# Performance work log

Hardware: AMD Instinct MI355X
Metric: run time of the kernel (lower is better)

The kernel has to match this reference:

```python
import jax, jax.numpy as jnp
import numpy as np

IN_CH = 512
MAX_MID = 512


def setup_inputs() -> dict:
    key = jax.random.key(0)
    k0, k1, k2, k3, k4 = jax.random.split(key, 5)
    B, C, H, W = 32, IN_CH, 64, 64
    x = jax.random.normal(k0, (B, C, H, W), dtype=jnp.float32)
    # torch.nn.Linear params: weight [out, in], bias [out]
    s1 = 1.0 / np.sqrt(C)
    w1 = jax.random.uniform(k1, (MAX_MID * 2, C), minval=-s1, maxval=s1, dtype=jnp.float32)
    b1 = jax.random.uniform(k2, (MAX_MID * 2,), minval=-s1, maxval=s1, dtype=jnp.float32)
    s2 = 1.0 / np.sqrt(MAX_MID * 2)
    w2 = jax.random.uniform(k3, (MAX_MID, MAX_MID * 2), minval=-s2, maxval=s2, dtype=jnp.float32)
    b2 = jax.random.uniform(k4, (MAX_MID,), minval=-s2, maxval=s2, dtype=jnp.float32)
    return {"x": x, "w1": w1, "b1": b1, "w2": w2, "b2": b2}


def reference(x, w1, b1, w2, b2):
    # Global average pool: [B, C, H, W] -> [B, C]
    gap = jnp.mean(x, axis=(2, 3))
    # Tiny 2-layer MLP: Linear -> ReLU -> Linear -> Sigmoid
    h = jax.nn.relu(gap @ w1.T + b1)
    scores = jax.nn.sigmoid(h @ w2.T + b2)  # [B, MAX_MID]
    B, M = scores.shape
    # Eval path: scale from mean score, clamped
    scale = jnp.clip(jnp.mean(scores), 0.25, 1.0)
    k_min = max(4, M // 4)
    k = jnp.clip(jnp.ceil(M * scale).astype(jnp.int32), k_min, M)  # scalar int
    # topk mask with dynamic k but static shapes: threshold = k-th largest per row
    sorted_desc = jnp.sort(scores, axis=1)[:, ::-1]  # [B, M] descending
    idx = jnp.full((B, 1), k - 1, dtype=jnp.int32)
    thresh = jnp.take_along_axis(sorted_desc, idx, axis=1)  # [B, 1]
    mask = (scores >= thresh).astype(scores.dtype)  # [B, M]
    return mask[:, :, None, None], k
```

## Files before the change

### kernel.cpp

```cpp
#include <hip/hip_runtime.h>

#define NB    32
#define CIN   512
#define MID2  1024
#define MID   512
#define HW    4096

__global__ __launch_bounds__(64) void k_gap(const float* __restrict__ x,
                                            float* __restrict__ gap) {
    const int row = blockIdx.x;
    const float4* x4 = (const float4*)(x + (size_t)row * HW);
    const int lane = threadIdx.x;
    float s0 = 0.f, s1 = 0.f, s2 = 0.f, s3 = 0.f;
#pragma unroll
    for (int it = 0; it < 4; ++it) {
        float4 a = x4[(4 * it + 0) * 64 + lane];
        float4 b = x4[(4 * it + 1) * 64 + lane];
        float4 c = x4[(4 * it + 2) * 64 + lane];
        float4 d = x4[(4 * it + 3) * 64 + lane];
        s0 += (a.x + a.y) + (a.z + a.w);
        s1 += (b.x + b.y) + (b.z + b.w);
        s2 += (c.x + c.y) + (c.z + c.w);
        s3 += (d.x + d.y) + (d.z + d.w);
    }
    float s = (s0 + s1) + (s2 + s3);
    for (int off = 32; off; off >>= 1) s += __shfl_down(s, off, 64);
    if (lane == 0) gap[row] = s * (1.0f / HW);
}

__global__ __launch_bounds__(256) void k_fc1(const float* __restrict__ gap,
                                             const float* __restrict__ w1,
                                             const float* __restrict__ b1,
                                             float* __restrict__ h) {
    const int wid = threadIdx.x >> 6, lane = threadIdx.x & 63;
    const int o = blockIdx.x * 4 + wid;
    const int b = o >> 10;
    const int j = o & (MID2 - 1);
    const float* g = gap + b * CIN;
    const float* w = w1 + (size_t)j * CIN;
    float s = 0.f;
#pragma unroll
    for (int i = 0; i < CIN / 64; ++i) {
        const int idx = i * 64 + lane;
        s += g[idx] * w[idx];
    }
    for (int off = 32; off; off >>= 1) s += __shfl_down(s, off, 64);
    if (lane == 0) h[o] = fmaxf(s + b1[j], 0.f);
}

__global__ __launch_bounds__(256) void k_fc2(const float* __restrict__ h,
                                             const float* __restrict__ w2,
                                             const float* __restrict__ b2,
                                             float* __restrict__ scores) {
    const int wid = threadIdx.x >> 6, lane = threadIdx.x & 63;
    const int o = blockIdx.x * 4 + wid;
    const int b = o >> 9;
    const int m = o & (MID - 1);
    const float* hh = h + b * MID2;
    const float* w = w2 + (size_t)m * MID2;
    float s = 0.f;
#pragma unroll
    for (int i = 0; i < MID2 / 64; ++i) {
        const int idx = i * 64 + lane;
        s += hh[idx] * w[idx];
    }
    for (int off = 32; off; off >>= 1) s += __shfl_down(s, off, 64);
    if (lane == 0) {
        const float v = s + b2[m];
        scores[o] = 1.0f / (1.0f + __expf(-v));
    }
}

__global__ __launch_bounds__(512) void k_mask(const float* __restrict__ scores,
                                              float* __restrict__ out) {
    __shared__ float srow[MID];
    __shared__ float red[8];
    __shared__ float thr;
    const int b = blockIdx.x, t = threadIdx.x;

    float s = 0.f;
#pragma unroll
    for (int i = 0; i < NB * MID / 512; ++i) s += scores[i * 512 + t];
    for (int off = 32; off; off >>= 1) s += __shfl_down(s, off, 64);
    const int wid = t >> 6, lane = t & 63;
    if (lane == 0) red[wid] = s;

    const float v = scores[b * MID + t];
    srow[t] = v;
    __syncthreads();

    const float tot = ((red[0] + red[1]) + (red[2] + red[3])) +
                      ((red[4] + red[5]) + (red[6] + red[7]));
    const float mean = tot / (float)(NB * MID);
    const float scale = fminf(fmaxf(mean, 0.25f), 1.0f);
    int k = (int)ceilf((float)MID * scale);
    k = min(max(k, 128), MID);

    const float4* srow4 = (const float4*)srow;
    int gt = 0, ge = 0;
    for (int i = 0; i < MID / 4; ++i) {
        const float4 u = srow4[i];
        gt += (u.x > v) + (u.y > v) + (u.z > v) + (u.w > v);
        ge += (u.x >= v) + (u.y >= v) + (u.z >= v) + (u.w >= v);
    }
    if (gt < k && ge >= k) thr = v;
    __syncthreads();
    out[b * MID + t] = (v >= thr) ? 1.0f : 0.0f;
    if (b == 0 && t == 0) out[NB * MID] = (float)k;
}

extern "C" void kernel_launch(void* const* d_in, const int* in_sizes, int n_in,
                              void* d_out, int out_size, void* d_ws, size_t ws_size,
                              hipStream_t stream) {
    const float* x  = (const float*)d_in[0];
    const float* w1 = (const float*)d_in[1];
    const float* b1 = (const float*)d_in[2];
    const float* w2 = (const float*)d_in[3];
    const float* b2 = (const float*)d_in[4];
    float* out = (float*)d_out;

    float* gap    = (float*)d_ws;
    float* h      = gap + NB * CIN;
    float* scores = h + NB * MID2;

    k_gap <<<NB * CIN,      64,  0, stream>>>(x, gap);
    k_fc1 <<<NB * MID2 / 4, 256, 0, stream>>>(gap, w1, b1, h);
    k_fc2 <<<NB * MID  / 4, 256, 0, stream>>>(h, w2, b2, scores);
    k_mask<<<NB,            512, 0, stream>>>(scores, out);
}
```

Before: 68.82 us.

## Fuse both MLP layers into one per-batch kernel and precompute score sums

```diff
diff --git a/kernel.cpp b/kernel.cpp
--- a/kernel.cpp
+++ b/kernel.cpp
@@ -6,11 +6,11 @@
 #define MID   512
 #define HW    4096
 
-__global__ __launch_bounds__(64) void k_gap(const float* __restrict__ x,
-                                            float* __restrict__ gap) {
-    const int row = blockIdx.x;
+__global__ __launch_bounds__(256) void k_gap(const float* __restrict__ x,
+                                             float* __restrict__ gap) {
+    const int row  = blockIdx.x * 4 + (threadIdx.x >> 6);
+    const int lane = threadIdx.x & 63;
     const float4* x4 = (const float4*)(x + (size_t)row * HW);
-    const int lane = threadIdx.x;
     float s0 = 0.f, s1 = 0.f, s2 = 0.f, s3 = 0.f;
 #pragma unroll
     for (int it = 0; it < 4; ++it) {
@@ -28,73 +28,87 @@
     if (lane == 0) gap[row] = s * (1.0f / HW);
 }
 
-__global__ __launch_bounds__(256) void k_fc1(const float* __restrict__ gap,
+__global__ __launch_bounds__(1024) void k_fc(const float* __restrict__ gap,
                                              const float* __restrict__ w1,
                                              const float* __restrict__ b1,
-                                             float* __restrict__ h) {
-    const int wid = threadIdx.x >> 6, lane = threadIdx.x & 63;
-    const int o = blockIdx.x * 4 + wid;
-    const int b = o >> 10;
-    const int j = o & (MID2 - 1);
-    const float* g = gap + b * CIN;
-    const float* w = w1 + (size_t)j * CIN;
-    float s = 0.f;
-#pragma unroll
-    for (int i = 0; i < CIN / 64; ++i) {
-        const int idx = i * 64 + lane;
-        s += g[idx] * w[idx];
-    }
-    for (int off = 32; off; off >>= 1) s += __shfl_down(s, off, 64);
-    if (lane == 0) h[o] = fmaxf(s + b1[j], 0.f);
-}
-
-__global__ __launch_bounds__(256) void k_fc2(const float* __restrict__ h,
                                              const float* __restrict__ w2,
                                              const float* __restrict__ b2,
-                                             float* __restrict__ scores) {
-    const int wid = threadIdx.x >> 6, lane = threadIdx.x & 63;
-    const int o = blockIdx.x * 4 + wid;
-    const int b = o >> 9;
-    const int m = o & (MID - 1);
-    const float* hh = h + b * MID2;
-    const float* w = w2 + (size_t)m * MID2;
-    float s = 0.f;
-#pragma unroll
-    for (int i = 0; i < MID2 / 64; ++i) {
-        const int idx = i * 64 + lane;
-        s += hh[idx] * w[idx];
+                                             float* __restrict__ scores,
+                                             float* __restrict__ sums) {
+    const int b = blockIdx.x;
+    const int t = threadIdx.x, wid = t >> 6, lane = t & 63;
+    __shared__ float hsh[MID2];
+    __shared__ float srow[MID];
+    __shared__ float red[8];
+
+    const float4 g0 = *(const float4*)(gap + b * CIN + lane * 8);
+    const float4 g1 = *(const float4*)(gap + b * CIN + lane * 8 + 4);
+
+#pragma unroll 2
+    for (int jo = 0; jo < 64; ++jo) {
+        const int j = wid * 64 + jo;
+        const float* w = w1 + (size_t)j * CIN + lane * 8;
+        const float4 a = *(const float4*)w;
+        const float4 c = *(const float4*)(w + 4);
+        float s = (a.x * g0.x + a.y * g0.y) + (a.z * g0.z + a.w * g0.w) +
+                  (c.x * g1.x + c.y * g1.y) + (c.z * g1.z + c.w * g1.w);
+        for (int off = 32; off; off >>= 1) s += __shfl_down(s, off, 64);
+        if (lane == 0) hsh[j] = fmaxf(s + b1[j], 0.f);
     }
-    for (int off = 32; off; off >>= 1) s += __shfl_down(s, off, 64);
-    if (lane == 0) {
-        const float v = s + b2[m];
-        scores[o] = 1.0f / (1.0f + __expf(-v));
+    __syncthreads();
+
+    const float4* h4 = (const float4*)(hsh + lane * 16);
+    const float4 h0 = h4[0], h1 = h4[1], h2 = h4[2], h3 = h4[3];
+
+#pragma unroll 2
+    for (int mo = 0; mo < 32; ++mo) {
+        const int m = wid * 32 + mo;
+        const float4* w = (const float4*)(w2 + (size_t)m * MID2 + lane * 16);
+        const float4 a = w[0], c = w[1], d = w[2], e = w[3];
+        float s = (a.x * h0.x + a.y * h0.y) + (a.z * h0.z + a.w * h0.w) +
+                  (c.x * h1.x + c.y * h1.y) + (c.z * h1.z + c.w * h1.w) +
+                  (d.x * h2.x + d.y * h2.y) + (d.z * h2.z + d.w * h2.w) +
+                  (e.x * h3.x + e.y * h3.y) + (e.z * h3.z + e.w * h3.w);
+        for (int off = 32; off; off >>= 1) s += __shfl_down(s, off, 64);
+        if (lane == 0) {
+            const float v = s + b2[m];
+            const float sc = 1.0f / (1.0f + __expf(-v));
+            srow[m] = sc;
+            scores[b * MID + m] = sc;
+        }
+    }
+    __syncthreads();
+
+    if (t < MID) {
+        float s = srow[t];
+        for (int off = 32; off; off >>= 1) s += __shfl_down(s, off, 64);
+        if (lane == 0) red[wid] = s;
+    }
+    __syncthreads();
+    if (t == 0) {
+        sums[b] = ((red[0] + red[1]) + (red[2] + red[3])) +
+                  ((red[4] + red[5]) + (red[6] + red[7]));
     }
 }
 
 __global__ __launch_bounds__(512) void k_mask(const float* __restrict__ scores,
+                                              const float* __restrict__ sums,
                                               float* __restrict__ out) {
     __shared__ float srow[MID];
-    __shared__ float red[8];
     __shared__ float thr;
     const int b = blockIdx.x, t = threadIdx.x;
 
-    float s = 0.f;
+    float tot = 0.f;
 #pragma unroll
-    for (int i = 0; i < NB * MID / 512; ++i) s += scores[i * 512 + t];
-    for (int off = 32; off; off >>= 1) s += __shfl_down(s, off, 64);
-    const int wid = t >> 6, lane = t & 63;
-    if (lane == 0) red[wid] = s;
+    for (int i = 0; i < NB; ++i) tot += sums[i];
+    const float mean = tot / (float)(NB * MID);
+    const float scale = fminf(fmaxf(mean, 0.25f), 1.0f);
+    int k = (int)ceilf((float)MID * scale);
+    k = min(max(k, 128), MID);
 
     const float v = scores[b * MID + t];
     srow[t] = v;
     __syncthreads();
-
-    const float tot = ((red[0] + red[1]) + (red[2] + red[3])) +
-                      ((red[4] + red[5]) + (red[6] + red[7]));
-    const float mean = tot / (float)(NB * MID);
-    const float scale = fminf(fmaxf(mean, 0.25f), 1.0f);
-    int k = (int)ceilf((float)MID * scale);
-    k = min(max(k, 128), MID);
 
     const float4* srow4 = (const float4*)srow;
     int gt = 0, ge = 0;
@@ -120,11 +134,10 @@
     float* out = (float*)d_out;
 
     float* gap    = (float*)d_ws;
-    float* h      = gap + NB * CIN;
-    float* scores = h + NB * MID2;
+    float* scores = gap + NB * CIN;
+    float* sums   = scores + NB * MID;
 
-    k_gap <<<NB * CIN,      64,  0, stream>>>(x, gap);
-    k_fc1 <<<NB * MID2 / 4, 256, 0, stream>>>(gap, w1, b1, h);
-    k_fc2 <<<NB * MID  / 4, 256, 0, stream>>>(h, w2, b2, scores);
-    k_mask<<<NB,            512, 0, stream>>>(scores, out);
+    k_gap <<<NB * CIN / 4, 256,  0, stream>>>(x, gap);
+    k_fc  <<<NB,           1024, 0, stream>>>(gap, w1, b1, w2, b2, scores, sums);
+    k_mask<<<NB,           512,  0, stream>>>(scores, sums, out);
 }
```

Measured after the change: 133.2 us. +93.6%, slower.
